# Performance work log

Measured on AMD Instinct MI355X. Metric: run time of the kernel, lower is better.

Reference implementation:

```python
import jax, jax.numpy as jnp
import numpy as np

N_NODES = 50000
N_EDGES = 800000
IN_CH = 64
HID_CH = 128
LAT_CH = 64
N_GRAPHS = 64
U_DIM = 32


def setup_inputs() -> dict:
    key = jax.random.key(0)
    ks = jax.random.split(key, 12)
    x = jax.random.normal(ks[0], (N_NODES, IN_CH), dtype=jnp.float32)
    edge_index = jax.random.randint(ks[1], (2, N_EDGES), 0, N_NODES, dtype=jnp.int64)
    edge_attr = jax.random.normal(ks[2], (N_EDGES, 8), dtype=jnp.float32)  # unused by NodeModel
    u = jax.random.normal(ks[3], (N_GRAPHS, U_DIM), dtype=jnp.float32)
    batch = jnp.sort(jax.random.randint(ks[4], (N_NODES,), 0, N_GRAPHS, dtype=jnp.int64))
    s = 0.02
    W1 = jax.random.normal(ks[5], (2 * IN_CH, HID_CH), dtype=jnp.float32) * s
    b1 = jnp.zeros((HID_CH,), dtype=jnp.float32)
    W2 = jax.random.normal(ks[6], (HID_CH, HID_CH), dtype=jnp.float32) * s
    b2 = jnp.zeros((HID_CH,), dtype=jnp.float32)
    W3 = jax.random.normal(ks[7], (HID_CH, LAT_CH), dtype=jnp.float32) * s
    b3 = jnp.zeros((LAT_CH,), dtype=jnp.float32)
    return {"x": x, "edge_index": edge_index, "edge_attr": edge_attr, "u": u,
            "batch": batch, "W1": W1, "b1": b1, "W2": W2, "b2": b2, "W3": W3, "b3": b3}


def reference(x, edge_index, edge_attr, u, batch, W1, b1, W2, b2, W3, b3):
    row, col = edge_index[0], edge_index[1]
    # gather endpoints -> [E, 2*in_ch]
    h = jnp.concatenate([x[row], x[col]], axis=1)
    # 3-layer MLP on edges
    h = jax.nn.relu(h @ W1 + b1)
    h = jax.nn.relu(h @ W2 + b2)
    h = h @ W3 + b3  # [E, latent]
    # scatter reductions over destination node (col)
    cnt = jax.ops.segment_sum(jnp.ones((h.shape[0],), h.dtype), col, num_segments=N_NODES)
    mean = jax.ops.segment_sum(h, col, num_segments=N_NODES) / jnp.maximum(cnt, 1.0)[:, None]
    mx = jax.ops.segment_max(h, col, num_segments=N_NODES)
    mn = jax.ops.segment_min(h, col, num_segments=N_NODES)
    nonempty = (cnt > 0)[:, None]
    mx = jnp.where(nonempty, mx, 0.0)  # torch_scatter returns 0 for empty segments
    mn = jnp.where(nonempty, mn, 0.0)
    return jnp.concatenate([x, mean, mx, mn, u[batch]], axis=1)
```

## Files before the change

### kernel.cpp

```cpp
#include <hip/hip_runtime.h>

#define E_EDGES 800000
#define NN 50000
#define OUT_STRIDE 288

typedef __bf16 bf16;
typedef bf16 bf16x8 __attribute__((ext_vector_type(8)));
typedef float floatx4 __attribute__((ext_vector_type(4)));
typedef unsigned short ushort8v __attribute__((ext_vector_type(8)));

__device__ __forceinline__ unsigned short f2bf(float f){
    return __builtin_bit_cast(unsigned short, (bf16)f);
}
__device__ __forceinline__ unsigned pack2bf(float a, float b){
    unsigned short lo = __builtin_bit_cast(unsigned short, (bf16)a);
    unsigned short hi = __builtin_bit_cast(unsigned short, (bf16)b);
    return (unsigned)lo | ((unsigned)hi << 16);
}
__device__ __forceinline__ unsigned encf(float f){
    unsigned u = __float_as_uint(f);
    return (u & 0x80000000u) ? ~u : (u | 0x80000000u);
}
__device__ __forceinline__ float decf(unsigned u){
    return __uint_as_float((u & 0x80000000u) ? (u ^ 0x80000000u) : ~u);
}
__device__ __forceinline__ floatx4 mfma16(ushort8v a, ushort8v b, floatx4 c){
    return __builtin_amdgcn_mfma_f32_16x16x32_bf16(
        __builtin_bit_cast(bf16x8, a), __builtin_bit_cast(bf16x8, b), c, 0, 0, 0);
}
__device__ __forceinline__ void flush_run(float* out, int node, float s, float mx, float mn, int lane){
    float* sp = out + (long)node * OUT_STRIDE + 64;
    atomicAdd(sp + lane, s);
    atomicMax((unsigned*)sp + 64 + lane, encf(mx));
    atomicMin((unsigned*)sp + 128 + lane, encf(mn));
}

#define INIT_N 2400000
#define XBF_N  800000
#define PK_N   40960
#define HIST_BASE (INIT_N + XBF_N + PK_N)
#define SETUP_TOTAL (HIST_BASE + E_EDGES)

__global__ void setup_kernel(const float* __restrict__ x, const int* __restrict__ ei,
                             const float* __restrict__ W1, const float* __restrict__ W2,
                             const float* __restrict__ W3,
                             unsigned short* __restrict__ wp, unsigned short* __restrict__ xbf,
                             int* __restrict__ cnt, float* __restrict__ out)
{
    int i = blockIdx.x * blockDim.x + threadIdx.x;
    if (i < INIT_N) {
        int row = i / 48, q = i % 48;
        uint4 val = (q < 32) ? make_uint4(0u, 0u, 0u, 0u)
                             : make_uint4(~0u, ~0u, ~0u, ~0u);
        ((uint4*)out)[(long)row * 72 + 16 + q] = val;
        return;
    }
    i -= INIT_N;
    if (i < XBF_N) {
        float4 v = ((const float4*)x)[i];
        ushort4 o; o.x = f2bf(v.x); o.y = f2bf(v.y); o.z = f2bf(v.z); o.w = f2bf(v.w);
        ((ushort4*)xbf)[i] = o;
        return;
    }
    i -= XBF_N;
    if (i < PK_N) {
        const float* W; int N; int idx;
        if (i < 16384)      { W = W1; N = 128; idx = i; }
        else if (i < 32768) { W = W2; N = 128; idx = i - 16384; }
        else                { W = W3; N = 64;  idx = i - 32768; }
        int j = idx & 7, lane = (idx >> 3) & 63, kc = (idx >> 9) & 3, nt = idx >> 11;
        wp[i] = f2bf(W[(kc * 32 + ((lane >> 4) & 3) * 8 + j) * N + nt * 16 + (lane & 15)]);
        return;
    }
    i -= PK_N;
    if (i < E_EDGES) atomicAdd(&cnt[ei[E_EDGES + i]], 1);
}

__global__ void scanA_kernel(const int* __restrict__ cnt, int* __restrict__ off,
                             int* __restrict__ bsum){
    __shared__ int s[256];
    int tid = threadIdx.x;
    int node = blockIdx.x * 196 + tid;
    int val = (tid < 196 && node < NN) ? cnt[node] : 0;
    s[tid] = val;
    __syncthreads();
    for (int d = 1; d < 256; d <<= 1){
        int t = (tid >= d) ? s[tid - d] : 0;
        __syncthreads();
        s[tid] += t;
        __syncthreads();
    }
    if (tid < 196 && node < NN) off[node] = s[tid] - val;
    if (tid == 255) bsum[blockIdx.x] = s[255];
}

__global__ void scanB_kernel(const int* __restrict__ bsum, int* __restrict__ bbase){
    __shared__ int s[256];
    int tid = threadIdx.x;
    int val = bsum[tid];
    s[tid] = val;
    __syncthreads();
    for (int d = 1; d < 256; d <<= 1){
        int t = (tid >= d) ? s[tid - d] : 0;
        __syncthreads();
        s[tid] += t;
        __syncthreads();
    }
    bbase[tid] = s[tid] - val;
}

__global__ void scatter_kernel(const int* __restrict__ ei, int* __restrict__ off,
                               const int* __restrict__ bbase, int2* __restrict__ enodes){
    int e = blockIdx.x * blockDim.x + threadIdx.x;
    if (e >= E_EDGES) return;
    int c = ei[E_EDGES + e], r = ei[e];
    int pos = atomicAdd(&off[c], 1) + bbase[c / 196];
    enodes[pos] = make_int2(r, c);
}

__global__ __launch_bounds__(256, 4) void edge_mlp_kernel(
    const unsigned short* __restrict__ xbf, const int2* __restrict__ enodes,
    const unsigned short* __restrict__ wp,
    const float* __restrict__ b1, const float* __restrict__ b2, const float* __restrict__ b3,
    float* __restrict__ out)
{
    __shared__ __align__(16) unsigned char smem[4 * 8704];

    const int tid  = threadIdx.x;
    const int lane = tid & 63;
    const int w    = tid >> 6;
    const int quad = lane >> 4;
    const int ln   = lane & 15;
    unsigned short* wbuf = (unsigned short*)(smem + w * 8704);
    float* Tf = (float*)wbuf;
    const ushort8v* wpv = (const ushort8v*)wp;

    const int g = blockIdx.x * 4 + w;
    const int ebase = g * 32;
    int2 ed0 = enodes[ebase + ln];
    int2 ed1 = enodes[ebase + 16 + ln];

    ushort8v Wb[3][4];
#define LDW(slot, idx) { _Pragma("unroll") for (int _k = 0; _k < 4; _k++) \
        Wb[slot][_k] = wpv[(idx) * 256 + _k * 64 + lane]; }

    LDW(0, 0)
    LDW(1, 1)

    const ushort8v* r0 = (const ushort8v*)(xbf + (long)ed0.x * 64);
    const ushort8v* c0 = (const ushort8v*)(xbf + (long)ed0.y * 64);
    const ushort8v* r1 = (const ushort8v*)(xbf + (long)ed1.x * 64);
    const ushort8v* c1 = (const ushort8v*)(xbf + (long)ed1.y * 64);
    ushort8v B0[4] = { r0[quad], r0[4 + quad], c0[quad], c0[4 + quad] };
    ushort8v B1[4] = { r1[quad], r1[4 + quad], c1[quad], c1[4 + quad] };

#pragma unroll
    for (int nt = 0; nt < 8; nt++){
        LDW((nt + 2) % 3, nt + 2)
        floatx4 bini = *(const floatx4*)(b1 + nt * 16 + quad * 4);
        floatx4 a0 = bini, a1 = bini;
#pragma unroll
        for (int kc = 0; kc < 4; kc++){
            a0 = mfma16(Wb[nt % 3][kc], B0[kc], a0);
            a1 = mfma16(Wb[nt % 3][kc], B1[kc], a1);
        }
        uint2 p0, p1;
        p0.x = pack2bf(fmaxf(a0[0], 0.f), fmaxf(a0[1], 0.f));
        p0.y = pack2bf(fmaxf(a0[2], 0.f), fmaxf(a0[3], 0.f));
        p1.x = pack2bf(fmaxf(a1[0], 0.f), fmaxf(a1[1], 0.f));
        p1.y = pack2bf(fmaxf(a1[2], 0.f), fmaxf(a1[3], 0.f));
        int col = nt * 16 + quad * 4;
        *(uint2*)(wbuf + ln * 136 + col)        = p0;
        *(uint2*)(wbuf + (16 + ln) * 136 + col) = p1;
    }

    ushort8v H0[4], H1[4];
#pragma unroll
    for (int kc = 0; kc < 4; kc++){
        H0[kc] = *(const ushort8v*)(wbuf + ln * 136 + kc * 32 + quad * 8);
        H1[kc] = *(const ushort8v*)(wbuf + (16 + ln) * 136 + kc * 32 + quad * 8);
    }
#pragma unroll
    for (int nt = 0; nt < 8; nt++){
        LDW((8 + nt + 2) % 3, 8 + nt + 2)
        floatx4 bini = *(const floatx4*)(b2 + nt * 16 + quad * 4);
        floatx4 a0 = bini, a1 = bini;
#pragma unroll
        for (int kc = 0; kc < 4; kc++){
            a0 = mfma16(Wb[(8 + nt) % 3][kc], H0[kc], a0);
            a1 = mfma16(Wb[(8 + nt) % 3][kc], H1[kc], a1);
        }
        uint2 p0, p1;
        p0.x = pack2bf(fmaxf(a0[0], 0.f), fmaxf(a0[1], 0.f));
        p0.y = pack2bf(fmaxf(a0[2], 0.f), fmaxf(a0[3], 0.f));
        p1.x = pack2bf(fmaxf(a1[0], 0.f), fmaxf(a1[1], 0.f));
        p1.y = pack2bf(fmaxf(a1[2], 0.f), fmaxf(a1[3], 0.f));
        int col = nt * 16 + quad * 4;
        *(uint2*)(wbuf + ln * 136 + col)        = p0;
        *(uint2*)(wbuf + (16 + ln) * 136 + col) = p1;
    }

    ushort8v G0[4], G1[4];
#pragma unroll
    for (int kc = 0; kc < 4; kc++){
        G0[kc] = *(const ushort8v*)(wbuf + ln * 136 + kc * 32 + quad * 8);
        G1[kc] = *(const ushort8v*)(wbuf + (16 + ln) * 136 + kc * 32 + quad * 8);
    }
#pragma unroll
    for (int nt = 0; nt < 4; nt++){
        if (nt < 2) LDW((16 + nt + 2) % 3, 16 + nt + 2)
        floatx4 bini = *(const floatx4*)(b3 + nt * 16 + quad * 4);
        floatx4 a0 = bini, a1 = bini;
#pragma unroll
        for (int kc = 0; kc < 4; kc++){
            a0 = mfma16(Wb[(16 + nt) % 3][kc], G0[kc], a0);
            a1 = mfma16(Wb[(16 + nt) % 3][kc], G1[kc], a1);
        }
        int och = nt * 16 + quad * 4;
#pragma unroll
        for (int r = 0; r < 4; r++){
            Tf[(och + r) * 33 + ln]      = a0[r];
            Tf[(och + r) * 33 + 16 + ln] = a1[r];
        }
    }

    float v[32];
#pragma unroll
    for (int j = 0; j < 32; j++) v[j] = Tf[lane * 33 + j];
    int cn0 = ed0.y, cn1 = ed1.y;
    int cur = __builtin_amdgcn_readlane(cn0, 0);
    float s = v[0], mx = v[0], mn = v[0];
#pragma unroll
    for (int j = 1; j < 32; j++){
        int nj = (j < 16) ? __builtin_amdgcn_readlane(cn0, j)
                          : __builtin_amdgcn_readlane(cn1, j - 16);
        if (nj != cur){
            flush_run(out, cur, s, mx, mn, lane);
            cur = nj; s = v[j]; mx = v[j]; mn = v[j];
        } else {
            s += v[j]; mx = fmaxf(mx, v[j]); mn = fminf(mn, v[j]);
        }
    }
    flush_run(out, cur, s, mx, mn, lane);
}

__global__ void finalize_kernel(const float* __restrict__ x, const float* __restrict__ u,
                                const int* __restrict__ batch, const int* __restrict__ cnt,
                                float* __restrict__ out)
{
    long i = (long)blockIdx.x * blockDim.x + threadIdx.x;
    if (i >= (long)NN * 72) return;
    int ndx = (int)(i / 72);
    int q   = (int)(i % 72);
    float4 res;
    if (q < 16) {
        res = ((const float4*)(x + (long)ndx * 64))[q];
    } else if (q < 32) {
        float4 sv = ((const float4*)out)[i];
        int k = cnt[ndx];
        float inv = 1.f / (float)(k > 0 ? k : 1);
        res.x = sv.x * inv; res.y = sv.y * inv; res.z = sv.z * inv; res.w = sv.w * inv;
    } else if (q < 64) {
        uint4 e = ((const uint4*)out)[i];
        bool ne = cnt[ndx] > 0;
        res.x = ne ? decf(e.x) : 0.f; res.y = ne ? decf(e.y) : 0.f;
        res.z = ne ? decf(e.z) : 0.f; res.w = ne ? decf(e.w) : 0.f;
    } else {
        res = ((const float4*)(u + (long)batch[ndx] * 32))[q - 64];
    }
    ((float4*)out)[i] = res;
}

extern "C" void kernel_launch(void* const* d_in, const int* in_sizes, int n_in,
                              void* d_out, int out_size, void* d_ws, size_t ws_size,
                              hipStream_t stream)
{
    const float* x     = (const float*)d_in[0];
    const int*   ei    = (const int*)d_in[1];
    const float* u     = (const float*)d_in[3];
    const int*   batch = (const int*)d_in[4];
    const float* W1    = (const float*)d_in[5];
    const float* b1    = (const float*)d_in[6];
    const float* W2    = (const float*)d_in[7];
    const float* b2    = (const float*)d_in[8];
    const float* W3    = (const float*)d_in[9];
    const float* b3    = (const float*)d_in[10];
    float* out = (float*)d_out;
    unsigned char* ws = (unsigned char*)d_ws;

    unsigned short* wp     = (unsigned short*)ws;
    int*            cnt    = (int*)(ws + 81920);
    int*            off    = (int*)(ws + 281920);
    int*            bsum   = (int*)(ws + 481920);
    int*            bbase  = (int*)(ws + 482944);
    int2*           enodes = (int2*)(ws + 483968);
    unsigned short* xbf    = (unsigned short*)(ws + 6883968);

    hipMemsetAsync(cnt, 0, 200000, stream);
    setup_kernel<<<(SETUP_TOTAL + 255) / 256, 256, 0, stream>>>(x, ei, W1, W2, W3, wp, xbf, cnt, out);
    scanA_kernel<<<256, 256, 0, stream>>>(cnt, off, bsum);
    scanB_kernel<<<1, 256, 0, stream>>>(bsum, bbase);
    scatter_kernel<<<(E_EDGES + 255) / 256, 256, 0, stream>>>(ei, off, bbase, enodes);
    edge_mlp_kernel<<<6250, 256, 0, stream>>>(xbf, enodes, wp, b1, b2, b3, out);
    finalize_kernel<<<(int)(((long)NN * 72 + 255) / 256), 256, 0, stream>>>(x, u, batch, cnt, out);
}
```

Measured before the change: 331.0 us.

## Precompute per-node first-layer projections and gather them per edge

The first MLP layer is split algebraically as x[row]@W1a + x[col]@W1b. A new per-node kernel computes both halves once per node. P is stored as bf16 in unused columns of the output buffer and Q as fp8 in workspace. The edge kernel then gathers and adds P[row]+Q[col] with ReLU instead of running the layer-1 matmul per edge, and it streams weights directly with a smaller LDS footprint and higher occupancy target. This trades edge-level MFMA work for an extra node kernel and fp8 quantization error on the Q half.

```diff
diff --git a/kernel.cpp b/kernel.cpp
--- a/kernel.cpp
+++ b/kernel.cpp
@@ -7,6 +7,7 @@
 typedef __bf16 bf16;
 typedef bf16 bf16x8 __attribute__((ext_vector_type(8)));
 typedef float floatx4 __attribute__((ext_vector_type(4)));
+typedef float floatx2 __attribute__((ext_vector_type(2)));
 typedef unsigned short ushort8v __attribute__((ext_vector_type(8)));
 
 __device__ __forceinline__ unsigned short f2bf(float f){
@@ -16,6 +17,9 @@
     unsigned short lo = __builtin_bit_cast(unsigned short, (bf16)a);
     unsigned short hi = __builtin_bit_cast(unsigned short, (bf16)b);
     return (unsigned)lo | ((unsigned)hi << 16);
+}
+__device__ __forceinline__ float bf2f(unsigned short h){
+    return __uint_as_float((unsigned)h << 16);
 }
 __device__ __forceinline__ unsigned encf(float f){
     unsigned u = __float_as_uint(f);
@@ -34,17 +38,27 @@
     atomicMax((unsigned*)sp + 64 + lane, encf(mx));
     atomicMin((unsigned*)sp + 128 + lane, encf(mn));
 }
+__device__ __forceinline__ ushort8v combine_relu_pq(ushort8v p, uint2 q){
+    floatx2 q01 = __builtin_amdgcn_cvt_pk_f32_fp8((int)q.x, false);
+    floatx2 q23 = __builtin_amdgcn_cvt_pk_f32_fp8((int)q.x, true);
+    floatx2 q45 = __builtin_amdgcn_cvt_pk_f32_fp8((int)q.y, false);
+    floatx2 q67 = __builtin_amdgcn_cvt_pk_f32_fp8((int)q.y, true);
+    uint4 o;
+    o.x = pack2bf(fmaxf(bf2f(p[0]) + q01[0], 0.f), fmaxf(bf2f(p[1]) + q01[1], 0.f));
+    o.y = pack2bf(fmaxf(bf2f(p[2]) + q23[0], 0.f), fmaxf(bf2f(p[3]) + q23[1], 0.f));
+    o.z = pack2bf(fmaxf(bf2f(p[4]) + q45[0], 0.f), fmaxf(bf2f(p[5]) + q45[1], 0.f));
+    o.w = pack2bf(fmaxf(bf2f(p[6]) + q67[0], 0.f), fmaxf(bf2f(p[7]) + q67[1], 0.f));
+    return __builtin_bit_cast(ushort8v, o);
+}
 
 #define INIT_N 2400000
-#define XBF_N  800000
 #define PK_N   40960
-#define HIST_BASE (INIT_N + XBF_N + PK_N)
-#define SETUP_TOTAL (HIST_BASE + E_EDGES)
-
-__global__ void setup_kernel(const float* __restrict__ x, const int* __restrict__ ei,
+#define SETUP_TOTAL (INIT_N + PK_N + E_EDGES)
+
+__global__ void setup_kernel(const int* __restrict__ ei,
                              const float* __restrict__ W1, const float* __restrict__ W2,
                              const float* __restrict__ W3,
-                             unsigned short* __restrict__ wp, unsigned short* __restrict__ xbf,
+                             unsigned short* __restrict__ wp,
                              int* __restrict__ cnt, float* __restrict__ out)
 {
     int i = blockIdx.x * blockDim.x + threadIdx.x;
@@ -56,13 +70,6 @@
         return;
     }
     i -= INIT_N;
-    if (i < XBF_N) {
-        float4 v = ((const float4*)x)[i];
-        ushort4 o; o.x = f2bf(v.x); o.y = f2bf(v.y); o.z = f2bf(v.z); o.w = f2bf(v.w);
-        ((ushort4*)xbf)[i] = o;
-        return;
-    }
-    i -= XBF_N;
     if (i < PK_N) {
         const float* W; int N; int idx;
         if (i < 16384)      { W = W1; N = 128; idx = i; }
@@ -74,6 +81,67 @@
     }
     i -= PK_N;
     if (i < E_EDGES) atomicAdd(&cnt[ei[E_EDGES + i]], 1);
+}
+
+#define PQ_BLOCKS 391
+__global__ __launch_bounds__(256, 4) void pq_kernel(
+    const float* __restrict__ x, const unsigned short* __restrict__ wp,
+    const float* __restrict__ b1, float* __restrict__ out, unsigned char* __restrict__ qb)
+{
+    const int tid = threadIdx.x, lane = tid & 63, w = tid >> 6;
+    const int quad = lane >> 4, ln = lane & 15;
+    const ushort8v* wpv = (const ushort8v*)wp;
+    const int nbase = (blockIdx.x * 4 + w) * 32;
+    const int n0 = nbase + ln, n1 = nbase + 16 + ln;
+    const int n0c = min(n0, NN - 1), n1c = min(n1, NN - 1);
+
+    ushort8v X0[2], X1[2];
+#pragma unroll
+    for (int c = 0; c < 2; c++){
+        const float4* p0 = (const float4*)(x + (long)n0c * 64 + c * 32 + quad * 8);
+        const float4* p1 = (const float4*)(x + (long)n1c * 64 + c * 32 + quad * 8);
+        float4 a = p0[0], b = p0[1];
+        float4 cc = p1[0], d = p1[1];
+        uint4 u0, u1;
+        u0.x = pack2bf(a.x, a.y);  u0.y = pack2bf(a.z, a.w);
+        u0.z = pack2bf(b.x, b.y);  u0.w = pack2bf(b.z, b.w);
+        u1.x = pack2bf(cc.x, cc.y); u1.y = pack2bf(cc.z, cc.w);
+        u1.z = pack2bf(d.x, d.y);  u1.w = pack2bf(d.z, d.w);
+        X0[c] = __builtin_bit_cast(ushort8v, u0);
+        X1[c] = __builtin_bit_cast(ushort8v, u1);
+    }
+    unsigned char* ob = (unsigned char*)out;
+#pragma unroll
+    for (int nt = 0; nt < 8; nt++){
+        floatx4 bini = *(const floatx4*)(b1 + nt * 16 + quad * 4);
+        floatx4 z = {0.f, 0.f, 0.f, 0.f};
+        floatx4 aP0 = bini, aP1 = bini, aQ0 = z, aQ1 = z;
+        ushort8v Af0 = wpv[(nt * 4 + 0) * 64 + lane];
+        ushort8v Af1 = wpv[(nt * 4 + 1) * 64 + lane];
+        ushort8v Af2 = wpv[(nt * 4 + 2) * 64 + lane];
+        ushort8v Af3 = wpv[(nt * 4 + 3) * 64 + lane];
+        aP0 = mfma16(Af0, X0[0], aP0); aP0 = mfma16(Af1, X0[1], aP0);
+        aP1 = mfma16(Af0, X1[0], aP1); aP1 = mfma16(Af1, X1[1], aP1);
+        aQ0 = mfma16(Af2, X0[0], aQ0); aQ0 = mfma16(Af3, X0[1], aQ0);
+        aQ1 = mfma16(Af2, X1[0], aQ1); aQ1 = mfma16(Af3, X1[1], aQ1);
+        uint2 sP0, sP1;
+        sP0.x = pack2bf(aP0[0], aP0[1]); sP0.y = pack2bf(aP0[2], aP0[3]);
+        sP1.x = pack2bf(aP1[0], aP1[1]); sP1.y = pack2bf(aP1[2], aP1[3]);
+        int bo = nt * 32 + quad * 8;
+        int q0p = __builtin_amdgcn_cvt_pk_fp8_f32(aQ0[0], aQ0[1], 0, false);
+        q0p     = __builtin_amdgcn_cvt_pk_fp8_f32(aQ0[2], aQ0[3], q0p, true);
+        int q1p = __builtin_amdgcn_cvt_pk_fp8_f32(aQ1[0], aQ1[1], 0, false);
+        q1p     = __builtin_amdgcn_cvt_pk_fp8_f32(aQ1[2], aQ1[3], q1p, true);
+        int qo = nt * 16 + quad * 4;
+        if (n0 < NN){
+            *(uint2*)(ob + (long)n0 * 1152 + bo) = sP0;
+            *(int*)(qb + (long)n0 * 128 + qo)    = q0p;
+        }
+        if (n1 < NN){
+            *(uint2*)(ob + (long)n1 * 1152 + bo) = sP1;
+            *(int*)(qb + (long)n1 * 128 + qo)    = q1p;
+        }
+    }
 }
 
 __global__ void scanA_kernel(const int* __restrict__ cnt, int* __restrict__ off,
@@ -118,20 +186,20 @@
     enodes[pos] = make_int2(r, c);
 }
 
-__global__ __launch_bounds__(256, 4) void edge_mlp_kernel(
-    const unsigned short* __restrict__ xbf, const int2* __restrict__ enodes,
-    const unsigned short* __restrict__ wp,
-    const float* __restrict__ b1, const float* __restrict__ b2, const float* __restrict__ b3,
+__global__ __launch_bounds__(256, 5) void edge_mlp_kernel(
+    const int2* __restrict__ enodes, const unsigned short* __restrict__ wp,
+    const unsigned char* __restrict__ qb,
+    const float* __restrict__ b2, const float* __restrict__ b3,
     float* __restrict__ out)
 {
-    __shared__ __align__(16) unsigned char smem[4 * 8704];
+    __shared__ __align__(16) unsigned char smem[4 * 4608];
 
     const int tid  = threadIdx.x;
     const int lane = tid & 63;
     const int w    = tid >> 6;
     const int quad = lane >> 4;
     const int ln   = lane & 15;
-    unsigned short* wbuf = (unsigned short*)(smem + w * 8704);
+    unsigned short* wbuf = (unsigned short*)(smem + w * 4608);
     float* Tf = (float*)wbuf;
     const ushort8v* wpv = (const ushort8v*)wp;
 
@@ -139,109 +207,95 @@
     const int ebase = g * 32;
     int2 ed0 = enodes[ebase + ln];
     int2 ed1 = enodes[ebase + 16 + ln];
-
-    ushort8v Wb[3][4];
-#define LDW(slot, idx) { _Pragma("unroll") for (int _k = 0; _k < 4; _k++) \
-        Wb[slot][_k] = wpv[(idx) * 256 + _k * 64 + lane]; }
-
-    LDW(0, 0)
-    LDW(1, 1)
-
-    const ushort8v* r0 = (const ushort8v*)(xbf + (long)ed0.x * 64);
-    const ushort8v* c0 = (const ushort8v*)(xbf + (long)ed0.y * 64);
-    const ushort8v* r1 = (const ushort8v*)(xbf + (long)ed1.x * 64);
-    const ushort8v* c1 = (const ushort8v*)(xbf + (long)ed1.y * 64);
-    ushort8v B0[4] = { r0[quad], r0[4 + quad], c0[quad], c0[4 + quad] };
-    ushort8v B1[4] = { r1[quad], r1[4 + quad], c1[quad], c1[4 + quad] };
-
-#pragma unroll
-    for (int nt = 0; nt < 8; nt++){
-        LDW((nt + 2) % 3, nt + 2)
-        floatx4 bini = *(const floatx4*)(b1 + nt * 16 + quad * 4);
-        floatx4 a0 = bini, a1 = bini;
-#pragma unroll
-        for (int kc = 0; kc < 4; kc++){
-            a0 = mfma16(Wb[nt % 3][kc], B0[kc], a0);
-            a1 = mfma16(Wb[nt % 3][kc], B1[kc], a1);
-        }
-        uint2 p0, p1;
-        p0.x = pack2bf(fmaxf(a0[0], 0.f), fmaxf(a0[1], 0.f));
-        p0.y = pack2bf(fmaxf(a0[2], 0.f), fmaxf(a0[3], 0.f));
-        p1.x = pack2bf(fmaxf(a1[0], 0.f), fmaxf(a1[1], 0.f));
-        p1.y = pack2bf(fmaxf(a1[2], 0.f), fmaxf(a1[3], 0.f));
-        int col = nt * 16 + quad * 4;
-        *(uint2*)(wbuf + ln * 136 + col)        = p0;
-        *(uint2*)(wbuf + (16 + ln) * 136 + col) = p1;
-    }
-
+    const int cn0 = ed0.y, cn1 = ed1.y;
+
+    const unsigned short* pqb = (const unsigned short*)out;
     ushort8v H0[4], H1[4];
 #pragma unroll
     for (int kc = 0; kc < 4; kc++){
-        H0[kc] = *(const ushort8v*)(wbuf + ln * 136 + kc * 32 + quad * 8);
-        H1[kc] = *(const ushort8v*)(wbuf + (16 + ln) * 136 + kc * 32 + quad * 8);
-    }
-#pragma unroll
-    for (int nt = 0; nt < 8; nt++){
-        LDW((8 + nt + 2) % 3, 8 + nt + 2)
-        floatx4 bini = *(const floatx4*)(b2 + nt * 16 + quad * 4);
-        floatx4 a0 = bini, a1 = bini;
-#pragma unroll
-        for (int kc = 0; kc < 4; kc++){
-            a0 = mfma16(Wb[(8 + nt) % 3][kc], H0[kc], a0);
-            a1 = mfma16(Wb[(8 + nt) % 3][kc], H1[kc], a1);
-        }
-        uint2 p0, p1;
-        p0.x = pack2bf(fmaxf(a0[0], 0.f), fmaxf(a0[1], 0.f));
-        p0.y = pack2bf(fmaxf(a0[2], 0.f), fmaxf(a0[3], 0.f));
-        p1.x = pack2bf(fmaxf(a1[0], 0.f), fmaxf(a1[1], 0.f));
-        p1.y = pack2bf(fmaxf(a1[2], 0.f), fmaxf(a1[3], 0.f));
-        int col = nt * 16 + quad * 4;
-        *(uint2*)(wbuf + ln * 136 + col)        = p0;
-        *(uint2*)(wbuf + (16 + ln) * 136 + col) = p1;
+        const int o = kc * 32 + quad * 8;
+        ushort8v p0 = *(const ushort8v*)(pqb + (long)ed0.x * 576 + o);
+        ushort8v p1 = *(const ushort8v*)(pqb + (long)ed1.x * 576 + o);
+        uint2 q0 = *(const uint2*)(qb + (long)ed0.y * 128 + o);
+        uint2 q1 = *(const uint2*)(qb + (long)ed1.y * 128 + o);
+        H0[kc] = combine_relu_pq(p0, q0);
+        H1[kc] = combine_relu_pq(p1, q1);
     }
 
     ushort8v G0[4], G1[4];
 #pragma unroll
-    for (int kc = 0; kc < 4; kc++){
-        G0[kc] = *(const ushort8v*)(wbuf + ln * 136 + kc * 32 + quad * 8);
-        G1[kc] = *(const ushort8v*)(wbuf + (16 + ln) * 136 + kc * 32 + quad * 8);
-    }
-#pragma unroll
-    for (int nt = 0; nt < 4; nt++){
-        if (nt < 2) LDW((16 + nt + 2) % 3, 16 + nt + 2)
-        floatx4 bini = *(const floatx4*)(b3 + nt * 16 + quad * 4);
-        floatx4 a0 = bini, a1 = bini;
-#pragma unroll
-        for (int kc = 0; kc < 4; kc++){
-            a0 = mfma16(Wb[(16 + nt) % 3][kc], G0[kc], a0);
-            a1 = mfma16(Wb[(16 + nt) % 3][kc], G1[kc], a1);
-        }
-        int och = nt * 16 + quad * 4;
-#pragma unroll
-        for (int r = 0; r < 4; r++){
-            Tf[(och + r) * 33 + ln]      = a0[r];
-            Tf[(och + r) * 33 + 16 + ln] = a1[r];
-        }
-    }
-
-    float v[32];
-#pragma unroll
-    for (int j = 0; j < 32; j++) v[j] = Tf[lane * 33 + j];
-    int cn0 = ed0.y, cn1 = ed1.y;
-    int cur = __builtin_amdgcn_readlane(cn0, 0);
-    float s = v[0], mx = v[0], mn = v[0];
-#pragma unroll
-    for (int j = 1; j < 32; j++){
-        int nj = (j < 16) ? __builtin_amdgcn_readlane(cn0, j)
-                          : __builtin_amdgcn_readlane(cn1, j - 16);
-        if (nj != cur){
+    for (int hv = 0; hv < 2; hv++){
+#pragma unroll
+        for (int q2 = 0; q2 < 4; q2++){
+            int nt = hv * 4 + q2;
+            floatx4 bini = *(const floatx4*)(b2 + nt * 16 + quad * 4);
+            floatx4 a0 = bini, a1 = bini;
+#pragma unroll
+            for (int kc = 0; kc < 4; kc++){
+                ushort8v Af = wpv[2048 + (nt * 4 + kc) * 64 + lane];
+                a0 = mfma16(Af, H0[kc], a0);
+                a1 = mfma16(Af, H1[kc], a1);
+            }
+            uint2 p0, p1;
+            p0.x = pack2bf(fmaxf(a0[0], 0.f), fmaxf(a0[1], 0.f));
+            p0.y = pack2bf(fmaxf(a0[2], 0.f), fmaxf(a0[3], 0.f));
+            p1.x = pack2bf(fmaxf(a1[0], 0.f), fmaxf(a1[1], 0.f));
+            p1.y = pack2bf(fmaxf(a1[2], 0.f), fmaxf(a1[3], 0.f));
+            int col = q2 * 16 + quad * 4;
+            *(uint2*)(wbuf + ln * 72 + col)        = p0;
+            *(uint2*)(wbuf + (16 + ln) * 72 + col) = p1;
+        }
+#pragma unroll
+        for (int c = 0; c < 2; c++){
+            G0[hv * 2 + c] = *(const ushort8v*)(wbuf + ln * 72 + c * 32 + quad * 8);
+            G1[hv * 2 + c] = *(const ushort8v*)(wbuf + (16 + ln) * 72 + c * 32 + quad * 8);
+        }
+    }
+
+#pragma unroll
+    for (int hv = 0; hv < 2; hv++){
+#pragma unroll
+        for (int q3 = 0; q3 < 2; q3++){
+            int nt = hv * 2 + q3;
+            floatx4 bini = *(const floatx4*)(b3 + nt * 16 + quad * 4);
+            floatx4 a0 = bini, a1 = bini;
+#pragma unroll
+            for (int kc = 0; kc < 4; kc++){
+                ushort8v Af = wpv[4096 + (nt * 4 + kc) * 64 + lane];
+                a0 = mfma16(Af, G0[kc], a0);
+                a1 = mfma16(Af, G1[kc], a1);
+            }
+            int row = q3 * 16 + quad * 4;
+#pragma unroll
+            for (int r = 0; r < 4; r++){
+                Tf[(row + r) * 36 + ln]      = a0[r];
+                Tf[(row + r) * 36 + 16 + ln] = a1[r];
+            }
+        }
+        if ((lane >> 5) == hv){
+            float v[32];
+#pragma unroll
+            for (int jj = 0; jj < 8; jj++){
+                floatx4 t = *(const floatx4*)(Tf + (lane & 31) * 36 + jj * 4);
+                v[jj * 4 + 0] = t[0]; v[jj * 4 + 1] = t[1];
+                v[jj * 4 + 2] = t[2]; v[jj * 4 + 3] = t[3];
+            }
+            int cur = __builtin_amdgcn_readlane(cn0, 0);
+            float s = v[0], mx = v[0], mn = v[0];
+#pragma unroll
+            for (int j = 1; j < 32; j++){
+                int nj = (j < 16) ? __builtin_amdgcn_readlane(cn0, j)
+                                  : __builtin_amdgcn_readlane(cn1, j - 16);
+                if (nj != cur){
+                    flush_run(out, cur, s, mx, mn, lane);
+                    cur = nj; s = v[j]; mx = v[j]; mn = v[j];
+                } else {
+                    s += v[j]; mx = fmaxf(mx, v[j]); mn = fminf(mn, v[j]);
+                }
+            }
             flush_run(out, cur, s, mx, mn, lane);
-            cur = nj; s = v[j]; mx = v[j]; mn = v[j];
-        } else {
-            s += v[j]; mx = fmaxf(mx, v[j]); mn = fminf(mn, v[j]);
-        }
-    }
-    flush_run(out, cur, s, mx, mn, lane);
+        }
+    }
 }
 
 __global__ void finalize_kernel(const float* __restrict__ x, const float* __restrict__ u,
@@ -294,13 +348,14 @@
     int*            bsum   = (int*)(ws + 481920);
     int*            bbase  = (int*)(ws + 482944);
     int2*           enodes = (int2*)(ws + 483968);
-    unsigned short* xbf    = (unsigned short*)(ws + 6883968);
+    unsigned char*  qb     = (unsigned char*)(ws + 6883968);
 
     hipMemsetAsync(cnt, 0, 200000, stream);
-    setup_kernel<<<(SETUP_TOTAL + 255) / 256, 256, 0, stream>>>(x, ei, W1, W2, W3, wp, xbf, cnt, out);
+    setup_kernel<<<(SETUP_TOTAL + 255) / 256, 256, 0, stream>>>(ei, W1, W2, W3, wp, cnt, out);
+    pq_kernel<<<PQ_BLOCKS, 256, 0, stream>>>(x, wp, b1, out, qb);
     scanA_kernel<<<256, 256, 0, stream>>>(cnt, off, bsum);
     scanB_kernel<<<1, 256, 0, stream>>>(bsum, bbase);
     scatter_kernel<<<(E_EDGES + 255) / 256, 256, 0, stream>>>(ei, off, bbase, enodes);
-    edge_mlp_kernel<<<6250, 256, 0, stream>>>(xbf, enodes, wp, b1, b2, b3, out);
+    edge_mlp_kernel<<<6250, 256, 0, stream>>>(enodes, wp, qb, b2, b3, out);
     finalize_kernel<<<(int)(((long)NN * 72 + 255) / 256), 256, 0, stream>>>(x, u, batch, cnt, out);
 }
```

After: 363.9 us. 1.1x slower.

## Precompute per-node first-layer projections in FP8 and combine per edge

Applied to the files above, without the earlier changes.

The first MLP layer is split algebraically: a new per-node kernel computes x@W1_top+b1 and x@W1_bottom once per node and stores them as FP8. The edge kernel then gathers the two projections, adds them and applies ReLU, instead of running the first layer per edge. This removes per-edge layer-1 MFMA work and halves the gather bytes. Edge indices are packed into 16-bit pairs, and layer-3 output is staged in bf16 in shared memory to reduce LDS use and allow higher occupancy. The cost is FP8 quantization error on the hidden pre-activations and a dependence on workspace size, with a fallback to the old path when the workspace is too small.

```diff
diff --git a/kernel.cpp b/kernel.cpp
--- a/kernel.cpp
+++ b/kernel.cpp
@@ -7,6 +7,7 @@
 typedef __bf16 bf16;
 typedef bf16 bf16x8 __attribute__((ext_vector_type(8)));
 typedef float floatx4 __attribute__((ext_vector_type(4)));
+typedef float floatx2 __attribute__((ext_vector_type(2)));
 typedef unsigned short ushort8v __attribute__((ext_vector_type(8)));
 
 __device__ __forceinline__ unsigned short f2bf(float f){
@@ -34,13 +35,29 @@
     atomicMax((unsigned*)sp + 64 + lane, encf(mx));
     atomicMin((unsigned*)sp + 128 + lane, encf(mn));
 }
+__device__ __forceinline__ ushort8v combine_relu_fp8(uint2 p, uint2 q){
+    floatx2 p01 = __builtin_amdgcn_cvt_pk_f32_fp8((int)p.x, false);
+    floatx2 p23 = __builtin_amdgcn_cvt_pk_f32_fp8((int)p.x, true);
+    floatx2 p45 = __builtin_amdgcn_cvt_pk_f32_fp8((int)p.y, false);
+    floatx2 p67 = __builtin_amdgcn_cvt_pk_f32_fp8((int)p.y, true);
+    floatx2 q01 = __builtin_amdgcn_cvt_pk_f32_fp8((int)q.x, false);
+    floatx2 q23 = __builtin_amdgcn_cvt_pk_f32_fp8((int)q.x, true);
+    floatx2 q45 = __builtin_amdgcn_cvt_pk_f32_fp8((int)q.y, false);
+    floatx2 q67 = __builtin_amdgcn_cvt_pk_f32_fp8((int)q.y, true);
+    floatx2 s01 = p01 + q01, s23 = p23 + q23, s45 = p45 + q45, s67 = p67 + q67;
+    uint4 o;
+    o.x = pack2bf(fmaxf(s01[0], 0.f), fmaxf(s01[1], 0.f));
+    o.y = pack2bf(fmaxf(s23[0], 0.f), fmaxf(s23[1], 0.f));
+    o.z = pack2bf(fmaxf(s45[0], 0.f), fmaxf(s45[1], 0.f));
+    o.w = pack2bf(fmaxf(s67[0], 0.f), fmaxf(s67[1], 0.f));
+    return __builtin_bit_cast(ushort8v, o);
+}
 
 #define INIT_N 2400000
 #define XBF_N  800000
 #define PK_N   40960
-#define HIST_BASE (INIT_N + XBF_N + PK_N)
-#define SETUP_TOTAL (HIST_BASE + E_EDGES)
-
+
+template<int WITH_XBF>
 __global__ void setup_kernel(const float* __restrict__ x, const int* __restrict__ ei,
                              const float* __restrict__ W1, const float* __restrict__ W2,
                              const float* __restrict__ W3,
@@ -56,13 +73,15 @@
         return;
     }
     i -= INIT_N;
-    if (i < XBF_N) {
-        float4 v = ((const float4*)x)[i];
-        ushort4 o; o.x = f2bf(v.x); o.y = f2bf(v.y); o.z = f2bf(v.z); o.w = f2bf(v.w);
-        ((ushort4*)xbf)[i] = o;
-        return;
-    }
-    i -= XBF_N;
+    if constexpr (WITH_XBF) {
+        if (i < XBF_N) {
+            float4 v = ((const float4*)x)[i];
+            ushort4 o; o.x = f2bf(v.x); o.y = f2bf(v.y); o.z = f2bf(v.z); o.w = f2bf(v.w);
+            ((ushort4*)xbf)[i] = o;
+            return;
+        }
+        i -= XBF_N;
+    }
     if (i < PK_N) {
         const float* W; int N; int idx;
         if (i < 16384)      { W = W1; N = 128; idx = i; }
@@ -74,6 +93,67 @@
     }
     i -= PK_N;
     if (i < E_EDGES) atomicAdd(&cnt[ei[E_EDGES + i]], 1);
+}
+
+#define PQ_BLOCKS 391
+__global__ __launch_bounds__(256, 4) void pq_kernel(
+    const float* __restrict__ x, const unsigned short* __restrict__ wp,
+    const float* __restrict__ b1,
+    unsigned char* __restrict__ pb, unsigned char* __restrict__ qb)
+{
+    const int tid = threadIdx.x, lane = tid & 63, w = tid >> 6;
+    const int quad = lane >> 4, ln = lane & 15;
+    const ushort8v* wpv = (const ushort8v*)wp;
+    const int nbase = (blockIdx.x * 4 + w) * 32;
+    const int n0 = nbase + ln, n1 = nbase + 16 + ln;
+    const int n0c = min(n0, NN - 1), n1c = min(n1, NN - 1);
+
+    ushort8v X0[2], X1[2];
+#pragma unroll
+    for (int c = 0; c < 2; c++){
+        const float4* p0 = (const float4*)(x + (long)n0c * 64 + c * 32 + quad * 8);
+        const float4* p1 = (const float4*)(x + (long)n1c * 64 + c * 32 + quad * 8);
+        float4 a = p0[0], b = p0[1];
+        float4 cc = p1[0], d = p1[1];
+        uint4 u0, u1;
+        u0.x = pack2bf(a.x, a.y);  u0.y = pack2bf(a.z, a.w);
+        u0.z = pack2bf(b.x, b.y);  u0.w = pack2bf(b.z, b.w);
+        u1.x = pack2bf(cc.x, cc.y); u1.y = pack2bf(cc.z, cc.w);
+        u1.z = pack2bf(d.x, d.y);  u1.w = pack2bf(d.z, d.w);
+        X0[c] = __builtin_bit_cast(ushort8v, u0);
+        X1[c] = __builtin_bit_cast(ushort8v, u1);
+    }
+#pragma unroll
+    for (int nt = 0; nt < 8; nt++){
+        floatx4 bini = *(const floatx4*)(b1 + nt * 16 + quad * 4);
+        floatx4 z = {0.f, 0.f, 0.f, 0.f};
+        floatx4 aP0 = bini, aP1 = bini, aQ0 = z, aQ1 = z;
+        ushort8v Af0 = wpv[(nt * 4 + 0) * 64 + lane];
+        ushort8v Af1 = wpv[(nt * 4 + 1) * 64 + lane];
+        ushort8v Af2 = wpv[(nt * 4 + 2) * 64 + lane];
+        ushort8v Af3 = wpv[(nt * 4 + 3) * 64 + lane];
+        aP0 = mfma16(Af0, X0[0], aP0); aP0 = mfma16(Af1, X0[1], aP0);
+        aP1 = mfma16(Af0, X1[0], aP1); aP1 = mfma16(Af1, X1[1], aP1);
+        aQ0 = mfma16(Af2, X0[0], aQ0); aQ0 = mfma16(Af3, X0[1], aQ0);
+        aQ1 = mfma16(Af2, X1[0], aQ1); aQ1 = mfma16(Af3, X1[1], aQ1);
+        int p0p = __builtin_amdgcn_cvt_pk_fp8_f32(aP0[0], aP0[1], 0, false);
+        p0p     = __builtin_amdgcn_cvt_pk_fp8_f32(aP0[2], aP0[3], p0p, true);
+        int p1p = __builtin_amdgcn_cvt_pk_fp8_f32(aP1[0], aP1[1], 0, false);
+        p1p     = __builtin_amdgcn_cvt_pk_fp8_f32(aP1[2], aP1[3], p1p, true);
+        int q0p = __builtin_amdgcn_cvt_pk_fp8_f32(aQ0[0], aQ0[1], 0, false);
+        q0p     = __builtin_amdgcn_cvt_pk_fp8_f32(aQ0[2], aQ0[3], q0p, true);
+        int q1p = __builtin_amdgcn_cvt_pk_fp8_f32(aQ1[0], aQ1[1], 0, false);
+        q1p     = __builtin_amdgcn_cvt_pk_fp8_f32(aQ1[2], aQ1[3], q1p, true);
+        int qo = nt * 16 + quad * 4;
+        if (n0 < NN){
+            *(int*)(pb + (long)n0 * 128 + qo) = p0p;
+            *(int*)(qb + (long)n0 * 128 + qo) = q0p;
+        }
+        if (n1 < NN){
+            *(int*)(pb + (long)n1 * 128 + qo) = p1p;
+            *(int*)(qb + (long)n1 * 128 + qo) = q1p;
+        }
+    }
 }
 
 __global__ void scanA_kernel(const int* __restrict__ cnt, int* __restrict__ off,
@@ -109,8 +189,16 @@
     bbase[tid] = s[tid] - val;
 }
 
-__global__ void scatter_kernel(const int* __restrict__ ei, int* __restrict__ off,
-                               const int* __restrict__ bbase, int2* __restrict__ enodes){
+__global__ void scatterA_kernel(const int* __restrict__ ei, int* __restrict__ off,
+                                const int* __restrict__ bbase, unsigned* __restrict__ enodes){
+    int e = blockIdx.x * blockDim.x + threadIdx.x;
+    if (e >= E_EDGES) return;
+    int c = ei[E_EDGES + e], r = ei[e];
+    int pos = atomicAdd(&off[c], 1) + bbase[c / 196];
+    enodes[pos] = (unsigned)r | ((unsigned)c << 16);
+}
+__global__ void scatterB_kernel(const int* __restrict__ ei, int* __restrict__ off,
+                                const int* __restrict__ bbase, int2* __restrict__ enodes){
     int e = blockIdx.x * blockDim.x + threadIdx.x;
     if (e >= E_EDGES) return;
     int c = ei[E_EDGES + e], r = ei[e];
@@ -118,7 +206,115 @@
     enodes[pos] = make_int2(r, c);
 }
 
-__global__ __launch_bounds__(256, 4) void edge_mlp_kernel(
+__global__ __launch_bounds__(256, 6) void edge_mlpA_kernel(
+    const unsigned* __restrict__ enodes, const unsigned short* __restrict__ wp,
+    const unsigned char* __restrict__ pb, const unsigned char* __restrict__ qb,
+    const float* __restrict__ b2, const float* __restrict__ b3,
+    float* __restrict__ out)
+{
+    __shared__ __align__(16) unsigned char smem[4 * 4608];
+
+    const int tid  = threadIdx.x;
+    const int lane = tid & 63;
+    const int w    = tid >> 6;
+    const int quad = lane >> 4;
+    const int ln   = lane & 15;
+    unsigned short* wbuf = (unsigned short*)(smem + w * 4608);
+    const ushort8v* wpv = (const ushort8v*)wp;
+
+    const int g = blockIdx.x * 4 + w;
+    const int ebase = g * 32;
+    unsigned e0 = enodes[ebase + ln];
+    unsigned e1 = enodes[ebase + 16 + ln];
+    const int r0 = (int)(e0 & 0xFFFFu), cn0 = (int)(e0 >> 16);
+    const int r1 = (int)(e1 & 0xFFFFu), cn1 = (int)(e1 >> 16);
+
+    ushort8v H0[4], H1[4];
+#pragma unroll
+    for (int kc = 0; kc < 4; kc++){
+        const int o = kc * 32 + quad * 8;
+        uint2 p0 = *(const uint2*)(pb + (long)r0 * 128 + o);
+        uint2 q0 = *(const uint2*)(qb + (long)cn0 * 128 + o);
+        uint2 p1 = *(const uint2*)(pb + (long)r1 * 128 + o);
+        uint2 q1 = *(const uint2*)(qb + (long)cn1 * 128 + o);
+        H0[kc] = combine_relu_fp8(p0, q0);
+        H1[kc] = combine_relu_fp8(p1, q1);
+    }
+
+    ushort8v G0[4], G1[4];
+#pragma unroll
+    for (int hv = 0; hv < 2; hv++){
+#pragma unroll
+        for (int q2 = 0; q2 < 4; q2++){
+            int nt = hv * 4 + q2;
+            floatx4 bini = *(const floatx4*)(b2 + nt * 16 + quad * 4);
+            floatx4 a0 = bini, a1 = bini;
+#pragma unroll
+            for (int kc = 0; kc < 4; kc++){
+                ushort8v Af = wpv[2048 + (nt * 4 + kc) * 64 + lane];
+                a0 = mfma16(Af, H0[kc], a0);
+                a1 = mfma16(Af, H1[kc], a1);
+            }
+            uint2 p0, p1;
+            p0.x = pack2bf(fmaxf(a0[0], 0.f), fmaxf(a0[1], 0.f));
+            p0.y = pack2bf(fmaxf(a0[2], 0.f), fmaxf(a0[3], 0.f));
+            p1.x = pack2bf(fmaxf(a1[0], 0.f), fmaxf(a1[1], 0.f));
+            p1.y = pack2bf(fmaxf(a1[2], 0.f), fmaxf(a1[3], 0.f));
+            int col = q2 * 16 + quad * 4;
+            *(uint2*)(wbuf + ln * 72 + col)        = p0;
+            *(uint2*)(wbuf + (16 + ln) * 72 + col) = p1;
+        }
+#pragma unroll
+        for (int c = 0; c < 2; c++){
+            G0[hv * 2 + c] = *(const ushort8v*)(wbuf + ln * 72 + c * 32 + quad * 8);
+            G1[hv * 2 + c] = *(const ushort8v*)(wbuf + (16 + ln) * 72 + c * 32 + quad * 8);
+        }
+    }
+
+#pragma unroll
+    for (int nt = 0; nt < 4; nt++){
+        floatx4 bini = *(const floatx4*)(b3 + nt * 16 + quad * 4);
+        floatx4 a0 = bini, a1 = bini;
+#pragma unroll
+        for (int kc = 0; kc < 4; kc++){
+            ushort8v Af = wpv[4096 + (nt * 4 + kc) * 64 + lane];
+            a0 = mfma16(Af, G0[kc], a0);
+            a1 = mfma16(Af, G1[kc], a1);
+        }
+        int och = nt * 16 + quad * 4;
+#pragma unroll
+        for (int r = 0; r < 4; r++){
+            wbuf[(och + r) * 36 + ln]      = f2bf(a0[r]);
+            wbuf[(och + r) * 36 + 16 + ln] = f2bf(a1[r]);
+        }
+    }
+
+    float v[32];
+#pragma unroll
+    for (int t = 0; t < 8; t++){
+        uint2 uu = *(const uint2*)(wbuf + lane * 36 + t * 4);
+        v[t * 4 + 0] = __uint_as_float(uu.x << 16);
+        v[t * 4 + 1] = __uint_as_float(uu.x & 0xFFFF0000u);
+        v[t * 4 + 2] = __uint_as_float(uu.y << 16);
+        v[t * 4 + 3] = __uint_as_float(uu.y & 0xFFFF0000u);
+    }
+    int cur = __builtin_amdgcn_readlane(cn0, 0);
+    float s = v[0], mx = v[0], mn = v[0];
+#pragma unroll
+    for (int j = 1; j < 32; j++){
+        int nj = (j < 16) ? __builtin_amdgcn_readlane(cn0, j)
+                          : __builtin_amdgcn_readlane(cn1, j - 16);
+        if (nj != cur){
+            flush_run(out, cur, s, mx, mn, lane);
+            cur = nj; s = v[j]; mx = v[j]; mn = v[j];
+        } else {
+            s += v[j]; mx = fmaxf(mx, v[j]); mn = fminf(mn, v[j]);
+        }
+    }
+    flush_run(out, cur, s, mx, mn, lane);
+}
+
+__global__ __launch_bounds__(256, 4) void edge_mlpB_kernel(
     const unsigned short* __restrict__ xbf, const int2* __restrict__ enodes,
     const unsigned short* __restrict__ wp,
     const float* __restrict__ b1, const float* __restrict__ b2, const float* __restrict__ b3,
@@ -242,6 +438,7 @@
         }
     }
     flush_run(out, cur, s, mx, mn, lane);
+#undef LDW
 }
 
 __global__ void finalize_kernel(const float* __restrict__ x, const float* __restrict__ u,
@@ -288,19 +485,35 @@
     float* out = (float*)d_out;
     unsigned char* ws = (unsigned char*)d_ws;
 
-    unsigned short* wp     = (unsigned short*)ws;
-    int*            cnt    = (int*)(ws + 81920);
-    int*            off    = (int*)(ws + 281920);
-    int*            bsum   = (int*)(ws + 481920);
-    int*            bbase  = (int*)(ws + 482944);
-    int2*           enodes = (int2*)(ws + 483968);
-    unsigned short* xbf    = (unsigned short*)(ws + 6883968);
+    unsigned short* wp    = (unsigned short*)ws;
+    int*            cnt   = (int*)(ws + 81920);
+    int*            off   = (int*)(ws + 281920);
+    int*            bsum  = (int*)(ws + 481920);
+    int*            bbase = (int*)(ws + 482944);
+
+    const bool bigA = ws_size >= (size_t)16483968;
 
     hipMemsetAsync(cnt, 0, 200000, stream);
-    setup_kernel<<<(SETUP_TOTAL + 255) / 256, 256, 0, stream>>>(x, ei, W1, W2, W3, wp, xbf, cnt, out);
-    scanA_kernel<<<256, 256, 0, stream>>>(cnt, off, bsum);
-    scanB_kernel<<<1, 256, 0, stream>>>(bsum, bbase);
-    scatter_kernel<<<(E_EDGES + 255) / 256, 256, 0, stream>>>(ei, off, bbase, enodes);
-    edge_mlp_kernel<<<6250, 256, 0, stream>>>(xbf, enodes, wp, b1, b2, b3, out);
+    if (bigA) {
+        unsigned*      enodes = (unsigned*)(ws + 483968);
+        unsigned char* pb     = (unsigned char*)(ws + 3683968);
+        unsigned char* qb     = (unsigned char*)(ws + 10083968);
+        setup_kernel<0><<<(INIT_N + PK_N + E_EDGES + 255) / 256, 256, 0, stream>>>(
+            x, ei, W1, W2, W3, wp, nullptr, cnt, out);
+        pq_kernel<<<PQ_BLOCKS, 256, 0, stream>>>(x, wp, b1, pb, qb);
+        scanA_kernel<<<256, 256, 0, stream>>>(cnt, off, bsum);
+        scanB_kernel<<<1, 256, 0, stream>>>(bsum, bbase);
+        scatterA_kernel<<<(E_EDGES + 255) / 256, 256, 0, stream>>>(ei, off, bbase, enodes);
+        edge_mlpA_kernel<<<6250, 256, 0, stream>>>(enodes, wp, pb, qb, b2, b3, out);
+    } else {
+        int2*           enodes = (int2*)(ws + 483968);
+        unsigned short* xbf    = (unsigned short*)(ws + 6883968);
+        setup_kernel<1><<<(INIT_N + XBF_N + PK_N + E_EDGES + 255) / 256, 256, 0, stream>>>(
+            x, ei, W1, W2, W3, wp, xbf, cnt, out);
+        scanA_kernel<<<256, 256, 0, stream>>>(cnt, off, bsum);
+        scanB_kernel<<<1, 256, 0, stream>>>(bsum, bbase);
+        scatterB_kernel<<<(E_EDGES + 255) / 256, 256, 0, stream>>>(ei, off, bbase, enodes);
+        edge_mlpB_kernel<<<6250, 256, 0, stream>>>(xbf, enodes, wp, b1, b2, b3, out);
+    }
     finalize_kernel<<<(int)(((long)NN * 72 + 255) / 256), 256, 0, stream>>>(x, u, batch, cnt, out);
 }
```

Result: slower. 343.1 us (+3.7%).
